# Performance work log

Hardware: AMD Instinct MI355X
Metric: run time of the kernel (lower is better)

The kernel has to match this reference:

```python
import jax, jax.numpy as jnp
import numpy as np

HEADS = 4
DIM_HEAD = 32
SCALE = DIM_HEAD ** -0.5

# Energy conventions (Hopfield / Lagrangian formulation):
#  Neuron(x): g = activation(x); e = sum(x*g) - L(x)
#  Synapse(g, x): e = -sum(g*x)
#  identity Lagrangian: L(x) = 0.5*sum(x^2), g = x  => Conv2d block energy = -0.5*sum(x^2)
#  softmax Lagrangian: L(x) = sum(logsumexp(x, -1)), g = softmax(x, -1)

def setup_inputs() -> dict:
    key = jax.random.key(0)
    ks = jax.random.split(key, 5)
    b, c, h, w = 8, 256, 48, 48
    hidden = HEADS * DIM_HEAD  # 128
    return {
        "x": jax.random.normal(ks[0], (b, c, h, w), jnp.float32),
        "w_qkv": jax.random.normal(ks[1], (hidden * 3, c), jnp.float32) * 0.02,
        "b_qkv": jax.random.normal(ks[2], (hidden * 3,), jnp.float32) * 0.02,
        "w_out": jax.random.normal(ks[3], (c, hidden), jnp.float32) * 0.02,
        "b_out": jax.random.normal(ks[4], (c,), jnp.float32) * 0.02,
    }

def reference(x, w_qkv, b_qkv, w_out, b_out):
    b, c, h, w = x.shape
    # 1x1 conv == channel matmul
    qkv = jnp.einsum('oc,bcxy->boxy', w_qkv, x) + b_qkv[None, :, None, None]
    e_qkv = -0.5 * jnp.sum(qkv * qkv)  # identity-Lagrangian neuron + synapse energy
    q, k, v = jnp.split(qkv, 3, axis=1)
    # 'b (h c) x y -> b h c (x y)'
    def heads(t):
        return t.reshape(b, HEADS, DIM_HEAD, h * w)
    q, k, v = heads(q), heads(k), heads(v)
    q = q * SCALE
    sim = jnp.einsum('bhdi,bhdj->bhij', q, k)  # [b, heads, hw, hw]
    sim = sim - jax.lax.stop_gradient(jnp.max(sim, axis=-1, keepdims=True))
    attn = jax.nn.softmax(sim, axis=-1)
    # softmax-Lagrangian neuron energy: sum(sim*attn) - sum(logsumexp(sim, -1))
    e_attn = jnp.sum(sim * attn) - jnp.sum(jax.nn.logsumexp(sim, axis=-1))
    out = jnp.einsum('bhij,bhdj->bhid', attn, v)  # [b, heads, hw, dim_head]
    # 'b h (x y) d -> b (h d) x y'
    out = out.transpose(0, 1, 3, 2).reshape(b, HEADS * DIM_HEAD, h, w)
    out = jnp.einsum('oc,bcxy->boxy', w_out, out) + b_out[None, :, None, None]
    e_out = -0.5 * jnp.sum(out * out)
    return out, e_attn + e_out + e_qkv
```

## Files before the change

### kernel.cpp

```cpp
#include <hip/hip_runtime.h>
#include <hip/hip_bf16.h>

#define HW 2304
#define NB 8
#define NC 256
#define HID 128
#define DH 32
#define NH 4
#define SCALE 0.17677669529663687f
#define LOG2E 1.4426950408889634f
#define LN2   0.6931471805599453f

using bf16x8 = __attribute__((ext_vector_type(8))) short;
using f32x4  = __attribute__((ext_vector_type(4))) float;

__device__ __forceinline__ short f2bf(float f) {
    unsigned u = __float_as_uint(f);
    u += 0x7FFF + ((u >> 16) & 1);
    return (short)(u >> 16);
}
__device__ __forceinline__ unsigned pk2bf(float a, float b) {
    union { __hip_bfloat162 h; unsigned u; } cv;
    cv.h = __float22bfloat162_rn(float2{a, b});
    return cv.u;
}
__device__ __forceinline__ void gld16(const void* g, void* l) {
    __builtin_amdgcn_global_load_lds(
        (const __attribute__((address_space(1))) unsigned*)g,
        (__attribute__((address_space(3))) unsigned*)l, 16, 0, 0);
}

__global__ __launch_bounds__(256)
void prep(const float* __restrict__ x, const float* __restrict__ wq,
          const float* __restrict__ wo, short* __restrict__ Xt,
          short* __restrict__ Wq, short* __restrict__ Wo, float* __restrict__ wsz)
{
    if (blockIdx.z == 8) {
        const int bid = blockIdx.x + 72 * blockIdx.y;
        if (bid == 0 && threadIdx.x == 0) { wsz[0] = 0.f; ((int*)wsz)[1] = 0; }
        const int i = bid * 256 + threadIdx.x;
        if (i < 384 * 256) Wq[i] = f2bf(wq[i]);
        if (i < 256 * 128) Wo[i] = f2bf(wo[i]);
        return;
    }
    __shared__ float T[32][33];
    const int b = blockIdx.z, c0 = blockIdx.y * 32, s0 = blockIdx.x * 32;
    const int ts = threadIdx.x & 31, tc = threadIdx.x >> 5;
    #pragma unroll
    for (int cc = tc; cc < 32; cc += 8)
        T[cc][ts] = x[((size_t)b * NC + c0 + cc) * HW + s0 + ts];
    __syncthreads();
    const int tcc = threadIdx.x & 31, tss = threadIdx.x >> 5;
    #pragma unroll
    for (int ss = tss; ss < 32; ss += 8)
        Xt[((size_t)b * HW + s0 + ss) * NC + c0 + tcc] = f2bf(T[tcc][ss]);
}

template<int KD, bool QKV>
__global__ __launch_bounds__(256, 4)
void conv_mfma(const short* __restrict__ A, const short* __restrict__ Bt,
               const float* __restrict__ bias, float* __restrict__ out0,
               short* __restrict__ Qb, short* __restrict__ Kb,
               short* __restrict__ Vb, float* __restrict__ E,
               int* __restrict__ ticket, int nblocks, float* __restrict__ edst)
{
    const int b  = blockIdx.z;
    const int bm = blockIdx.y * 64;
    const int bn = blockIdx.x * 128;
    const int t  = threadIdx.x;
    const int w  = t >> 6, lane = t & 63;
    const int n16 = lane & 15, quad = lane >> 4;

    __shared__ __align__(16) char csm[24576];
    __shared__ float red[4];

    const int rL = lane >> 2, cswz = (lane & 3) ^ (rL & 3);
    const char* agl = (const char*)(A  + (size_t)(bm + rL) * KD + cswz * 8);
    const char* bgl = (const char*)(Bt + ((size_t)b * HW + bn + rL) * KD + cswz * 8);

    auto issue = [&](int kc, int pbuf) {
        char* base = csm + pbuf * 12288;
        if (w == 0) {
            gld16(agl + (size_t)(0 * 16 * KD + kc) * 2, base + 0 * 1024);
            gld16(agl + (size_t)(1 * 16 * KD + kc) * 2, base + 1 * 1024);
            gld16(bgl + (size_t)(0 * 16 * KD + kc) * 2, base + 4096 + 0 * 1024);
        } else if (w == 1) {
            gld16(agl + (size_t)(2 * 16 * KD + kc) * 2, base + 2 * 1024);
            gld16(agl + (size_t)(3 * 16 * KD + kc) * 2, base + 3 * 1024);
            gld16(bgl + (size_t)(1 * 16 * KD + kc) * 2, base + 4096 + 1 * 1024);
        } else if (w == 2) {
            gld16(bgl + (size_t)(2 * 16 * KD + kc) * 2, base + 4096 + 2 * 1024);
            gld16(bgl + (size_t)(3 * 16 * KD + kc) * 2, base + 4096 + 3 * 1024);
            gld16(bgl + (size_t)(4 * 16 * KD + kc) * 2, base + 4096 + 4 * 1024);
        } else {
            gld16(bgl + (size_t)(5 * 16 * KD + kc) * 2, base + 4096 + 5 * 1024);
            gld16(bgl + (size_t)(6 * 16 * KD + kc) * 2, base + 4096 + 6 * 1024);
            gld16(bgl + (size_t)(7 * 16 * KD + kc) * 2, base + 4096 + 7 * 1024);
        }
    };

    f32x4 acc[4][2] = {};
    const int rsw = (quad ^ (n16 & 3)) * 16;
    constexpr int NI = KD / 32;

    issue(0, 0);
    for (int ki = 0; ki < NI; ++ki) {
        const int p = ki & 1;
        __syncthreads();
        if (ki + 1 < NI) issue((ki + 1) * 32, p ^ 1);

        const char* Ap = csm + p * 12288;
        const char* Bp = Ap + 4096;
        bf16x8 am[4], bq[2];
        #pragma unroll
        for (int tm = 0; tm < 4; ++tm)
            am[tm] = *(const bf16x8*)(Ap + tm * 1024 + n16 * 64 + rsw);
        #pragma unroll
        for (int j = 0; j < 2; ++j)
            bq[j] = *(const bf16x8*)(Bp + (w * 2 + j) * 1024 + n16 * 64 + rsw);
        #pragma unroll
        for (int tm = 0; tm < 4; ++tm)
            #pragma unroll
            for (int j = 0; j < 2; ++j)
                acc[tm][j] = __builtin_amdgcn_mfma_f32_16x16x32_bf16(am[tm], bq[j], acc[tm][j], 0, 0, 0);
    }

    float e = 0.f;
    #pragma unroll
    for (int tm = 0; tm < 4; ++tm) {
        const int o0 = bm + tm * 16 + quad * 4;
        const float4 bb = *(const float4*)(bias + o0);
        #pragma unroll
        for (int j = 0; j < 2; ++j) {
            const int s = bn + (w * 2 + j) * 16 + n16;
            float v[4] = {acc[tm][j][0] + bb.x, acc[tm][j][1] + bb.y,
                          acc[tm][j][2] + bb.z, acc[tm][j][3] + bb.w};
            e -= 0.5f * (v[0]*v[0] + v[1]*v[1] + v[2]*v[2] + v[3]*v[3]);
            if (QKV) {
                if (o0 < HID) {
                    const int h = o0 >> 5, dh0 = o0 & 31;
                    const float qs = SCALE * LOG2E;
                    short4 pk = {f2bf(v[0]*qs), f2bf(v[1]*qs),
                                 f2bf(v[2]*qs), f2bf(v[3]*qs)};
                    *(short4*)(Qb + ((size_t)(b * NH + h) * HW + s) * DH + dh0) = pk;
                } else if (o0 < 2 * HID) {
                    const int c = o0 - HID, h = c >> 5, dh0 = c & 31;
                    const int g = s & 31;
                    const int sp = (s & ~31) | ((g & 1) << 4) | (g >> 1);
                    short4 pk = {f2bf(v[0]), f2bf(v[1]), f2bf(v[2]), f2bf(v[3])};
                    *(short4*)(Kb + ((size_t)(b * NH + h) * HW + sp) * DH + dh0) = pk;
                } else {
                    const int c = o0 - 2 * HID, h = c >> 5, dh0 = c & 31;
                    #pragma unroll
                    for (int r = 0; r < 4; ++r)
                        Vb[((size_t)(b * NH + h) * DH + dh0 + r) * HW + s] = f2bf(v[r]);
                }
            } else {
                #pragma unroll
                for (int r = 0; r < 4; ++r)
                    out0[((size_t)b * NC + o0 + r) * HW + s] = v[r];
            }
        }
    }

    #pragma unroll
    for (int off = 32; off > 0; off >>= 1) e += __shfl_down(e, off);
    if (lane == 0) red[w] = e;
    __syncthreads();
    if (t == 0) {
        atomicAdd(E, red[0] + red[1] + red[2] + red[3]);
        if (!QKV) {
            __threadfence();
            const int prev = atomicAdd(ticket, 1);
            if (prev == nblocks - 1) {
                __threadfence();
                edst[0] = atomicAdd(E, 0.f);
            }
        }
    }
}

__global__ __launch_bounds__(256)
void flash7(const short* __restrict__ Qb, const short* __restrict__ Kb,
            const short* __restrict__ Vb, short* __restrict__ attT,
            float* __restrict__ E)
{
    __shared__ __align__(16) char smem[16384 + 4 * 5120];

    const int bh   = blockIdx.y;
    const int w    = threadIdx.x >> 6;
    const int lane = threadIdx.x & 63;
    const int n16  = lane & 15, quad = lane >> 4;
    const int qb   = blockIdx.x * 128 + w * 32;

    bf16x8 aq[2];
    #pragma unroll
    for (int qg = 0; qg < 2; ++qg)
        aq[qg] = *(const bf16x8*)(Qb + ((size_t)bh * HW + qb + qg * 16 + n16) * DH + quad * 8);

    const int rL = lane >> 2, cL = (lane & 3) ^ (rL & 3);
    const char* gbase; size_t gstep;
    if (w < 2) {
        gbase = (const char*)(Kb + (size_t)bh * HW * DH) + ((w & 1) * 16 + rL) * 64 + cL * 16;
        gstep = 2048;
    } else {
        gbase = (const char*)(Vb + (size_t)bh * DH * HW)
              + (size_t)((w & 1) * 16 + rL) * (HW * 2) + cL * 16;
        gstep = 64;
    }

    gld16(gbase,         smem + 0    + w * 1024);
    gld16(gbase + gstep, smem + 4096 + w * 1024);

    f32x4 acc[2][2] = {};
    float ls[2][4] = {}, ts[2][4] = {};
    const int swz = (quad ^ (n16 & 3)) * 8;
    short* Pbase = (short*)(smem + 16384) + w * 2560;

    for (int it = 0; it < 36; ++it) {
        const int p = it & 1;
        __syncthreads();
        if (it + 1 < 36) {
            const size_t g0 = (size_t)(2 * it + 2) * gstep;
            gld16(gbase + g0,         smem + (p ^ 1) * 8192 + 0    + w * 1024);
            gld16(gbase + g0 + gstep, smem + (p ^ 1) * 8192 + 4096 + w * 1024);
        }

        #pragma unroll
        for (int ca = 0; ca < 2; ++ca) {
            const short* kb = (const short*)(smem + p * 8192 + ca * 4096);
            short* Ps = Pbase + ca * 1280;
            unsigned* P32 = (unsigned*)Ps;

            const bf16x8 bk0 = *(const bf16x8*)(kb + n16 * 32 + swz);
            const bf16x8 bk1 = *(const bf16x8*)(kb + 512  + n16 * 32 + swz);
            const bf16x8 bv0 = *(const bf16x8*)(kb + 1024 + n16 * 32 + swz);
            const bf16x8 bv1 = *(const bf16x8*)(kb + 1536 + n16 * 32 + swz);

            #pragma unroll
            for (int qg = 0; qg < 2; ++qg) {
                f32x4 z = {};
                const f32x4 s0 = __builtin_amdgcn_mfma_f32_16x16x32_bf16(aq[qg], bk0, z, 0, 0, 0);
                const f32x4 s1 = __builtin_amdgcn_mfma_f32_16x16x32_bf16(aq[qg], bk1, z, 0, 0, 0);
                #pragma unroll
                for (int r = 0; r < 4; ++r) {
                    const float p0 = __builtin_amdgcn_exp2f(s0[r]);
                    const float p1 = __builtin_amdgcn_exp2f(s1[r]);
                    ls[qg][r] += p0 + p1;
                    ts[qg][r] += p0 * s0[r] + p1 * s1[r];
                    P32[(qg * 16 + quad * 4 + r) * 20 + n16] = pk2bf(p0, p1);
                }
            }
            #pragma unroll
            for (int qg = 0; qg < 2; ++qg) {
                const bf16x8 pa = *(const bf16x8*)(Ps + (qg * 16 + n16) * 40 + quad * 8);
                acc[qg][0] = __builtin_amdgcn_mfma_f32_16x16x32_bf16(pa, bv0, acc[qg][0], 0, 0, 0);
                acc[qg][1] = __builtin_amdgcn_mfma_f32_16x16x32_bf16(pa, bv1, acc[qg][1], 0, 0, 0);
            }
        }
    }

    #pragma unroll
    for (int m = 1; m < 16; m <<= 1)
        #pragma unroll
        for (int qg = 0; qg < 2; ++qg)
            #pragma unroll
            for (int r = 0; r < 4; ++r) {
                ls[qg][r] += __shfl_xor(ls[qg][r], m);
                ts[qg][r] += __shfl_xor(ts[qg][r], m);
            }

    const int bb = bh >> 2, h = bh & 3;
    float e = 0.f;
    #pragma unroll
    for (int qg = 0; qg < 2; ++qg)
        #pragma unroll
        for (int r = 0; r < 4; ++r) {
            const int q = qb + qg * 16 + quad * 4 + r;
            const float L = ls[qg][r];
            const float invl = 1.f / L;
            short* ap = attT + ((size_t)bb * HW + q) * HID + h * 32;
            ap[n16]      = f2bf(acc[qg][0][r] * invl);
            ap[n16 + 16] = f2bf(acc[qg][1][r] * invl);
            e += (LN2 * ts[qg][r]) * invl - __logf(L);
        }
    e = (n16 == 0) ? e : 0.f;
    e += __shfl_xor(e, 16);
    e += __shfl_xor(e, 32);
    if (lane == 0) atomicAdd(E, e);
}

extern "C" void kernel_launch(void* const* d_in, const int* in_sizes, int n_in,
                              void* d_out, int out_size, void* d_ws, size_t ws_size,
                              hipStream_t stream) {
    const float* x     = (const float*)d_in[0];
    const float* w_qkv = (const float*)d_in[1];
    const float* b_qkv = (const float*)d_in[2];
    const float* w_out = (const float*)d_in[3];
    const float* b_out = (const float*)d_in[4];
    float* out = (float*)d_out;

    float* wsf    = (float*)d_ws;
    float* E      = wsf;
    int*   ticket = (int*)d_ws + 1;
    short* Xt   = (short*)(wsf + 16);
    short* Wq   = Xt + (size_t)NB * HW * NC;
    short* Wo   = Wq + 384 * 256;
    short* Qb   = Wo + 256 * 128;
    short* Kb   = Qb + (size_t)NB * NH * HW * DH;
    short* Vb   = Kb + (size_t)NB * NH * HW * DH;
    short* attT = Vb + (size_t)NB * NH * HW * DH;

    prep<<<dim3(HW / 32, NC / 32, NB + 1), 256, 0, stream>>>(
        x, w_qkv, w_out, Xt, Wq, Wo, wsf);
    conv_mfma<NC, true><<<dim3(18, 6, NB), 256, 0, stream>>>(
        Wq, Xt, b_qkv, nullptr, Qb, Kb, Vb, E, nullptr, 0, nullptr);
    flash7<<<dim3(HW / 128, NB * NH), 256, 0, stream>>>(
        Qb, Kb, Vb, attT, E);
    conv_mfma<HID, false><<<dim3(18, 4, NB), 256, 0, stream>>>(
        Wo, attT, b_out, out, nullptr, nullptr, nullptr, E,
        ticket, 18 * 4 * NB, out + (size_t)NB * NC * HW);
}
```

Measured before the change: 210.4 us.

## Split attention key range across two blocks with in-kernel partial merge

The flash attention kernel now splits each query tile's key range in half across two blocks, doubling grid size from 576 to 1152 blocks to fill more CUs. The first block to finish writes its bf16 partial output and row sums to a scratch buffer (reusing the Xt region) and signals a flag. The second block spin-waits on that flag, merges the partials and writes the final result and energy. This adds a spin-wait whose progress depends on the first block having run, a bf16 rounding of the partial accumulators, and extra global traffic.

```diff
diff --git a/kernel.cpp b/kernel.cpp
--- a/kernel.cpp
+++ b/kernel.cpp
@@ -10,6 +10,10 @@
 #define SCALE 0.17677669529663687f
 #define LOG2E 1.4426950408889634f
 #define LN2   0.6931471805599453f
+#define NQT 18
+#define KSPL 2
+#define KHALF (HW / KSPL)
+#define NIT (KHALF / 64)
 
 using bf16x8 = __attribute__((ext_vector_type(8))) short;
 using f32x4  = __attribute__((ext_vector_type(4))) float;
@@ -38,6 +42,10 @@
     if (blockIdx.z == 8) {
         const int bid = blockIdx.x + 72 * blockIdx.y;
         if (bid == 0 && threadIdx.x == 0) { wsz[0] = 0.f; ((int*)wsz)[1] = 0; }
+        if (bid < 5) {
+            const int i2 = bid * 256 + threadIdx.x;
+            if (i2 < 2 * NQT * 32) ((int*)wsz)[16 + i2] = 0;
+        }
         const int i = bid * 256 + threadIdx.x;
         if (i < 384 * 256) Wq[i] = f2bf(wq[i]);
         if (i < 256 * 128) Wo[i] = f2bf(wo[i]);
@@ -181,17 +189,21 @@
 }
 
 __global__ __launch_bounds__(256)
-void flash7(const short* __restrict__ Qb, const short* __restrict__ Kb,
+void flash8(const short* __restrict__ Qb, const short* __restrict__ Kb,
             const short* __restrict__ Vb, short* __restrict__ attT,
-            float* __restrict__ E)
+            float* __restrict__ E, int* __restrict__ ftk, int* __restrict__ frd,
+            char* __restrict__ part)
 {
     __shared__ __align__(16) char smem[16384 + 4 * 5120];
-
+    __shared__ int sprev;
+
+    const int qt   = blockIdx.x >> 1, kh = blockIdx.x & 1;
     const int bh   = blockIdx.y;
     const int w    = threadIdx.x >> 6;
     const int lane = threadIdx.x & 63;
     const int n16  = lane & 15, quad = lane >> 4;
-    const int qb   = blockIdx.x * 128 + w * 32;
+    const int qb   = qt * 128 + w * 32;
+    const int pidx = bh * NQT + qt;
 
     bf16x8 aq[2];
     #pragma unroll
@@ -199,12 +211,14 @@
         aq[qg] = *(const bf16x8*)(Qb + ((size_t)bh * HW + qb + qg * 16 + n16) * DH + quad * 8);
 
     const int rL = lane >> 2, cL = (lane & 3) ^ (rL & 3);
+    const int kbeg = kh * KHALF;
     const char* gbase; size_t gstep;
     if (w < 2) {
-        gbase = (const char*)(Kb + (size_t)bh * HW * DH) + ((w & 1) * 16 + rL) * 64 + cL * 16;
+        gbase = (const char*)(Kb + ((size_t)bh * HW + kbeg) * DH)
+              + ((w & 1) * 16 + rL) * 64 + cL * 16;
         gstep = 2048;
     } else {
-        gbase = (const char*)(Vb + (size_t)bh * DH * HW)
+        gbase = (const char*)(Vb + (size_t)bh * DH * HW + kbeg)
               + (size_t)((w & 1) * 16 + rL) * (HW * 2) + cL * 16;
         gstep = 64;
     }
@@ -217,10 +231,10 @@
     const int swz = (quad ^ (n16 & 3)) * 8;
     short* Pbase = (short*)(smem + 16384) + w * 2560;
 
-    for (int it = 0; it < 36; ++it) {
+    for (int it = 0; it < NIT; ++it) {
         const int p = it & 1;
         __syncthreads();
-        if (it + 1 < 36) {
+        if (it + 1 < NIT) {
             const size_t g0 = (size_t)(2 * it + 2) * gstep;
             gld16(gbase + g0,         smem + (p ^ 1) * 8192 + 0    + w * 1024);
             gld16(gbase + g0 + gstep, smem + (p ^ 1) * 8192 + 4096 + w * 1024);
@@ -270,19 +284,54 @@
                 ts[qg][r] += __shfl_xor(ts[qg][r], m);
             }
 
+    char* pb = part + (size_t)pidx * 9216;
+    unsigned* O32 = (unsigned*)pb;
+    float* pls = (float*)(pb + 8192);
+    float* pts = pls + 128;
+
+    if (threadIdx.x == 0) sprev = atomicAdd(&ftk[pidx], 1);
+    __syncthreads();
+    const int prev = sprev;
+
+    if (prev == 0) {
+        #pragma unroll
+        for (int qg = 0; qg < 2; ++qg)
+            #pragma unroll
+            for (int r = 0; r < 4; ++r) {
+                const int ql = w * 32 + qg * 16 + quad * 4 + r;
+                O32[ql * 16 + n16] = pk2bf(acc[qg][0][r], acc[qg][1][r]);
+                if (n16 == 0) { pls[ql] = ls[qg][r]; pts[ql] = ts[qg][r]; }
+            }
+        __threadfence();
+        __syncthreads();
+        if (threadIdx.x == 0) atomicExch(&frd[pidx], 1);
+        return;
+    }
+
+    if (threadIdx.x == 0) {
+        while (atomicCAS(&frd[pidx], 2, 2) != 1) __builtin_amdgcn_s_sleep(8);
+    }
+    __syncthreads();
+    __threadfence();
+
     const int bb = bh >> 2, h = bh & 3;
     float e = 0.f;
     #pragma unroll
     for (int qg = 0; qg < 2; ++qg)
         #pragma unroll
         for (int r = 0; r < 4; ++r) {
-            const int q = qb + qg * 16 + quad * 4 + r;
-            const float L = ls[qg][r];
+            const int ql = w * 32 + qg * 16 + quad * 4 + r;
+            const unsigned u = O32[ql * 16 + n16];
+            float a0 = acc[qg][0][r] + __uint_as_float(u << 16);
+            float a1 = acc[qg][1][r] + __uint_as_float(u & 0xffff0000u);
+            const float L = ls[qg][r] + pls[ql];
+            const float T = ts[qg][r] + pts[ql];
             const float invl = 1.f / L;
+            const int q = qt * 128 + ql;
             short* ap = attT + ((size_t)bb * HW + q) * HID + h * 32;
-            ap[n16]      = f2bf(acc[qg][0][r] * invl);
-            ap[n16 + 16] = f2bf(acc[qg][1][r] * invl);
-            e += (LN2 * ts[qg][r]) * invl - __logf(L);
+            ap[n16]      = f2bf(a0 * invl);
+            ap[n16 + 16] = f2bf(a1 * invl);
+            e += (LN2 * T) * invl - __logf(L);
         }
     e = (n16 == 0) ? e : 0.f;
     e += __shfl_xor(e, 16);
@@ -303,20 +352,23 @@
     float* wsf    = (float*)d_ws;
     float* E      = wsf;
     int*   ticket = (int*)d_ws + 1;
-    short* Xt   = (short*)(wsf + 16);
-    short* Wq   = Xt + (size_t)NB * HW * NC;
+    int*   ftk    = (int*)d_ws + 16;
+    int*   frd    = ftk + NQT * 32;
+    short* Wq   = (short*)(wsf + 1280);
     short* Wo   = Wq + 384 * 256;
-    short* Qb   = Wo + 256 * 128;
+    short* Xt   = Wo + 256 * 128;
+    short* Qb   = Xt + (size_t)NB * HW * NC;
     short* Kb   = Qb + (size_t)NB * NH * HW * DH;
     short* Vb   = Kb + (size_t)NB * NH * HW * DH;
     short* attT = Vb + (size_t)NB * NH * HW * DH;
+    char*  part = (char*)Xt;
 
     prep<<<dim3(HW / 32, NC / 32, NB + 1), 256, 0, stream>>>(
         x, w_qkv, w_out, Xt, Wq, Wo, wsf);
     conv_mfma<NC, true><<<dim3(18, 6, NB), 256, 0, stream>>>(
         Wq, Xt, b_qkv, nullptr, Qb, Kb, Vb, E, nullptr, 0, nullptr);
-    flash7<<<dim3(HW / 128, NB * NH), 256, 0, stream>>>(
-        Qb, Kb, Vb, attT, E);
+    flash8<<<dim3(NQT * KSPL, NB * NH), 256, 0, stream>>>(
+        Qb, Kb, Vb, attT, E, ftk, frd, part);
     conv_mfma<HID, false><<<dim3(18, 4, NB), 256, 0, stream>>>(
         Wo, attT, b_out, out, nullptr, nullptr, nullptr, E,
         ticket, 18 * 4 * NB, out + (size_t)NB * NC * HW);
```

Measured after the change: 307.1 us. 46.0% more time.

## Split attention over key halves with atomic partial sums and separate normalize kernel

Applied to the files above, without the earlier changes.

The flash attention kernel now splits the key range in two, doubling the grid from 576 to 1152 blocks so more CUs stay busy. Partial unnormalized outputs and row sums are combined with float atomics into zeroed fp32 buffers. A new norm_att kernel then normalizes, converts to bf16 and computes the softmax energy term. This adds a memset, an extra kernel launch, fp32 atomic traffic and a round trip through an fp32 intermediate. The P staging buffer per wave is also halved so less LDS is used, which may allow more resident blocks.

```diff
diff --git a/kernel.cpp b/kernel.cpp
--- a/kernel.cpp
+++ b/kernel.cpp
@@ -10,6 +10,10 @@
 #define SCALE 0.17677669529663687f
 #define LOG2E 1.4426950408889634f
 #define LN2   0.6931471805599453f
+#define NQT 18
+#define KSPL 2
+#define KHALF (HW / KSPL)
+#define NIT (KHALF / 64)
 
 using bf16x8 = __attribute__((ext_vector_type(8))) short;
 using f32x4  = __attribute__((ext_vector_type(4))) float;
@@ -181,17 +185,18 @@
 }
 
 __global__ __launch_bounds__(256)
-void flash7(const short* __restrict__ Qb, const short* __restrict__ Kb,
-            const short* __restrict__ Vb, short* __restrict__ attT,
-            float* __restrict__ E)
+void flash9(const short* __restrict__ Qb, const short* __restrict__ Kb,
+            const short* __restrict__ Vb, float* __restrict__ attO,
+            float* __restrict__ Lb, float* __restrict__ Tb)
 {
-    __shared__ __align__(16) char smem[16384 + 4 * 5120];
-
+    __shared__ __align__(16) char smem[16384 + 4 * 2560];
+
+    const int qt   = blockIdx.x >> 1, kh = blockIdx.x & 1;
     const int bh   = blockIdx.y;
     const int w    = threadIdx.x >> 6;
     const int lane = threadIdx.x & 63;
     const int n16  = lane & 15, quad = lane >> 4;
-    const int qb   = blockIdx.x * 128 + w * 32;
+    const int qb   = qt * 128 + w * 32;
 
     bf16x8 aq[2];
     #pragma unroll
@@ -199,12 +204,14 @@
         aq[qg] = *(const bf16x8*)(Qb + ((size_t)bh * HW + qb + qg * 16 + n16) * DH + quad * 8);
 
     const int rL = lane >> 2, cL = (lane & 3) ^ (rL & 3);
+    const int kbeg = kh * KHALF;
     const char* gbase; size_t gstep;
     if (w < 2) {
-        gbase = (const char*)(Kb + (size_t)bh * HW * DH) + ((w & 1) * 16 + rL) * 64 + cL * 16;
+        gbase = (const char*)(Kb + ((size_t)bh * HW + kbeg) * DH)
+              + ((w & 1) * 16 + rL) * 64 + cL * 16;
         gstep = 2048;
     } else {
-        gbase = (const char*)(Vb + (size_t)bh * DH * HW)
+        gbase = (const char*)(Vb + (size_t)bh * DH * HW + kbeg)
               + (size_t)((w & 1) * 16 + rL) * (HW * 2) + cL * 16;
         gstep = 64;
     }
@@ -215,12 +222,13 @@
     f32x4 acc[2][2] = {};
     float ls[2][4] = {}, ts[2][4] = {};
     const int swz = (quad ^ (n16 & 3)) * 8;
-    short* Pbase = (short*)(smem + 16384) + w * 2560;
-
-    for (int it = 0; it < 36; ++it) {
+    short* Ps = (short*)(smem + 16384) + w * 1280;
+    unsigned* P32 = (unsigned*)Ps;
+
+    for (int it = 0; it < NIT; ++it) {
         const int p = it & 1;
         __syncthreads();
-        if (it + 1 < 36) {
+        if (it + 1 < NIT) {
             const size_t g0 = (size_t)(2 * it + 2) * gstep;
             gld16(gbase + g0,         smem + (p ^ 1) * 8192 + 0    + w * 1024);
             gld16(gbase + g0 + gstep, smem + (p ^ 1) * 8192 + 4096 + w * 1024);
@@ -229,8 +237,6 @@
         #pragma unroll
         for (int ca = 0; ca < 2; ++ca) {
             const short* kb = (const short*)(smem + p * 8192 + ca * 4096);
-            short* Ps = Pbase + ca * 1280;
-            unsigned* P32 = (unsigned*)Ps;
 
             const bf16x8 bk0 = *(const bf16x8*)(kb + n16 * 32 + swz);
             const bf16x8 bk1 = *(const bf16x8*)(kb + 512  + n16 * 32 + swz);
@@ -271,23 +277,60 @@
             }
 
     const int bb = bh >> 2, h = bh & 3;
-    float e = 0.f;
     #pragma unroll
     for (int qg = 0; qg < 2; ++qg)
         #pragma unroll
         for (int r = 0; r < 4; ++r) {
             const int q = qb + qg * 16 + quad * 4 + r;
-            const float L = ls[qg][r];
-            const float invl = 1.f / L;
-            short* ap = attT + ((size_t)bb * HW + q) * HID + h * 32;
-            ap[n16]      = f2bf(acc[qg][0][r] * invl);
-            ap[n16 + 16] = f2bf(acc[qg][1][r] * invl);
-            e += (LN2 * ts[qg][r]) * invl - __logf(L);
-        }
-    e = (n16 == 0) ? e : 0.f;
-    e += __shfl_xor(e, 16);
-    e += __shfl_xor(e, 32);
-    if (lane == 0) atomicAdd(E, e);
+            float* op = attO + ((size_t)bb * HW + q) * HID + h * 32;
+            atomicAdd(op + n16,      acc[qg][0][r]);
+            atomicAdd(op + n16 + 16, acc[qg][1][r]);
+        }
+    if (n16 == 0) {
+        #pragma unroll
+        for (int qg = 0; qg < 2; ++qg)
+            #pragma unroll
+            for (int r = 0; r < 4; ++r) {
+                const int q = qb + qg * 16 + quad * 4 + r;
+                atomicAdd(&Lb[(size_t)bh * HW + q], ls[qg][r]);
+                atomicAdd(&Tb[(size_t)bh * HW + q], ts[qg][r]);
+            }
+    }
+}
+
+__global__ __launch_bounds__(256)
+void norm_att(const float* __restrict__ attO, const float* __restrict__ Lb,
+              const float* __restrict__ Tb, short* __restrict__ attT,
+              float* __restrict__ E)
+{
+    __shared__ float red[4];
+    const int b  = blockIdx.y;
+    const int s  = blockIdx.x * 16 + (threadIdx.x >> 4);
+    const int c0 = (threadIdx.x & 15) * 8;
+    const int h  = c0 >> 5;
+
+    const float L = Lb[((size_t)(b * NH + h)) * HW + s];
+    const float invl = 1.f / L;
+    const float* op = attO + ((size_t)b * HW + s) * HID + c0;
+    const float4 v0 = *(const float4*)(op);
+    const float4 v1 = *(const float4*)(op + 4);
+    unsigned* ap = (unsigned*)(attT + ((size_t)b * HW + s) * HID + c0);
+    ap[0] = pk2bf(v0.x * invl, v0.y * invl);
+    ap[1] = pk2bf(v0.z * invl, v0.w * invl);
+    ap[2] = pk2bf(v1.x * invl, v1.y * invl);
+    ap[3] = pk2bf(v1.z * invl, v1.w * invl);
+
+    float e = 0.f;
+    if ((c0 & 31) == 0) {
+        const float T = Tb[((size_t)(b * NH + h)) * HW + s];
+        e = (LN2 * T) * invl - __logf(L);
+    }
+    #pragma unroll
+    for (int off = 32; off > 0; off >>= 1) e += __shfl_down(e, off);
+    const int lane = threadIdx.x & 63;
+    if (lane == 0) red[threadIdx.x >> 6] = e;
+    __syncthreads();
+    if (threadIdx.x == 0) atomicAdd(E, red[0] + red[1] + red[2] + red[3]);
 }
 
 extern "C" void kernel_launch(void* const* d_in, const int* in_sizes, int n_in,
@@ -303,20 +346,28 @@
     float* wsf    = (float*)d_ws;
     float* E      = wsf;
     int*   ticket = (int*)d_ws + 1;
-    short* Xt   = (short*)(wsf + 16);
-    short* Wq   = Xt + (size_t)NB * HW * NC;
+    short* Wq   = (short*)(wsf + 16);
     short* Wo   = Wq + 384 * 256;
-    short* Qb   = Wo + 256 * 128;
+    short* Xt   = Wo + 256 * 128;
+    short* Qb   = Xt + (size_t)NB * HW * NC;
     short* Kb   = Qb + (size_t)NB * NH * HW * DH;
     short* Vb   = Kb + (size_t)NB * NH * HW * DH;
     short* attT = Vb + (size_t)NB * NH * HW * DH;
+    float* attO = (float*)(attT + (size_t)NB * HW * HID);
+    float* Lb   = attO + (size_t)NB * HW * HID;
+    float* Tb   = Lb + (size_t)NB * NH * HW;
+
+    const size_t zbytes = ((size_t)NB * HW * HID + 2 * (size_t)NB * NH * HW) * 4;
+    (void)hipMemsetAsync(attO, 0, zbytes, stream);
 
     prep<<<dim3(HW / 32, NC / 32, NB + 1), 256, 0, stream>>>(
         x, w_qkv, w_out, Xt, Wq, Wo, wsf);
     conv_mfma<NC, true><<<dim3(18, 6, NB), 256, 0, stream>>>(
         Wq, Xt, b_qkv, nullptr, Qb, Kb, Vb, E, nullptr, 0, nullptr);
-    flash7<<<dim3(HW / 128, NB * NH), 256, 0, stream>>>(
-        Qb, Kb, Vb, attT, E);
+    flash9<<<dim3(NQT * KSPL, NB * NH), 256, 0, stream>>>(
+        Qb, Kb, Vb, attO, Lb, Tb);
+    norm_att<<<dim3(HW / 16, NB), 256, 0, stream>>>(
+        attO, Lb, Tb, attT, E);
     conv_mfma<HID, false><<<dim3(18, 4, NB), 256, 0, stream>>>(
         Wo, attT, b_out, out, nullptr, nullptr, nullptr, E,
         ticket, 18 * 4 * NB, out + (size_t)NB * NC * HW);
```

Result: slower. 214.6 us (+2.0%).
